# Performance work log

Measured on AMD Instinct MI355X. Metric: run time of the kernel, lower is better.

## Reference

```python
import jax, jax.numpy as jnp
import numpy as np

DROPOUT_P = 0.5
HALF_D_LOG_2PI = 8.0  # 0.5 * D * log(2*pi) constant from source, D=16


def _dropout(key, x, p):
    keep = 1.0 - p
    mask = jax.random.bernoulli(key, keep, x.shape).astype(x.dtype)
    return x * mask / keep


def _spmm(adj_vals, row, col, support, n):
    # out[i] = sum_{e: row[e]==i} adj_vals[e] * support[col[e]]
    return jax.ops.segment_sum(adj_vals[:, None] * support[col], row, num_segments=n)


def setup_inputs() -> dict:
    key = jax.random.key(0)
    ks = jax.random.split(key, 9)
    N, F_IN, D, C, E, K = 100000, 512, 16, 16, 3200000, 16
    return {
        "x": jax.random.normal(ks[0], (N, F_IN), dtype=jnp.float32),
        "W1": jax.random.normal(ks[1], (F_IN, D), dtype=jnp.float32) * 0.05,
        "W2": jax.random.normal(ks[2], (D, C), dtype=jnp.float32) * 0.2,
        "adj_vals": jax.random.uniform(ks[3], (E,), dtype=jnp.float32),
        "PI": jax.random.uniform(ks[4], (K,), dtype=jnp.float32, minval=0.01, maxval=1.0),
        "MUs": jax.random.normal(ks[5], (K, D), dtype=jnp.float32),
        "PREs": jax.random.uniform(ks[6], (K, D), dtype=jnp.float32, minval=0.1, maxval=1.0),
        "row": jnp.sort(jax.random.randint(ks[7], (E,), 0, N, dtype=jnp.int32)),
        "col": jax.random.randint(ks[8], (E,), 0, N, dtype=jnp.int32),
    }


def reference(x, W1, W2, adj_vals, PI, MUs, PREs, row, col):
    n = x.shape[0]
    dk1, dk2 = jax.random.split(jax.random.key(42))
    # layer 1: dropout -> linear (P1) -> spmm (P2)
    h = _spmm(adj_vals, row, col, _dropout(dk1, x, DROPOUT_P) @ W1, n)  # [N, D]
    # GMM log-likelihood: log N(h | MU_k, diag(1/PRE_k)) + log PI_k
    diff = h[:, None, :] - MUs[None, :, :]                      # [N, K, D]
    logcomp = (-0.5 * jnp.sum(diff * diff * PREs[None], axis=2)
               + jnp.log(PI)[None, :]
               + 0.5 * jnp.sum(jnp.log(PREs), axis=1)[None, :]
               - HALF_D_LOG_2PI * jnp.log(2.0 * jnp.pi))        # [N, K]
    probs = -jnp.mean(jnp.max(logcomp, axis=1))
    # layer 2: relu -> dropout -> linear -> spmm -> log_softmax
    x1 = jax.nn.relu(h)
    h2 = _spmm(adj_vals, row, col, _dropout(dk2, x1, DROPOUT_P) @ W2, n)  # [N, C]
    return jax.nn.log_softmax(h2, axis=1), probs
```

## Files before the change

### kernel.cpp

```cpp
#include <hip/hip_runtime.h>
#include <stdint.h>

typedef __attribute__((ext_vector_type(8))) short bf16x8;
typedef __attribute__((ext_vector_type(4))) float f32x4;
typedef __attribute__((ext_vector_type(4))) int i32x4;

__host__ __device__ __forceinline__ uint32_t rotl32(uint32_t x, int d){
  return (x << d) | (x >> (32 - d));
}

__host__ __device__ __forceinline__ void threefry2x32(uint32_t k0, uint32_t k1,
                                                      uint32_t x0, uint32_t x1,
                                                      uint32_t* o0, uint32_t* o1){
  uint32_t ks2 = k0 ^ k1 ^ 0x1BD11BDAu;
  x0 += k0; x1 += k1;
  x0 += x1; x1 = rotl32(x1,13); x1 ^= x0;
  x0 += x1; x1 = rotl32(x1,15); x1 ^= x0;
  x0 += x1; x1 = rotl32(x1,26); x1 ^= x0;
  x0 += x1; x1 = rotl32(x1, 6); x1 ^= x0;
  x0 += k1; x1 += ks2 + 1u;
  x0 += x1; x1 = rotl32(x1,17); x1 ^= x0;
  x0 += x1; x1 = rotl32(x1,29); x1 ^= x0;
  x0 += x1; x1 = rotl32(x1,16); x1 ^= x0;
  x0 += x1; x1 = rotl32(x1,24); x1 ^= x0;
  x0 += ks2; x1 += k0 + 2u;
  x0 += x1; x1 = rotl32(x1,13); x1 ^= x0;
  x0 += x1; x1 = rotl32(x1,15); x1 ^= x0;
  x0 += x1; x1 = rotl32(x1,26); x1 ^= x0;
  x0 += x1; x1 = rotl32(x1, 6); x1 ^= x0;
  x0 += k0; x1 += k1 + 3u;
  x0 += x1; x1 = rotl32(x1,17); x1 ^= x0;
  x0 += x1; x1 = rotl32(x1,29); x1 ^= x0;
  x0 += x1; x1 = rotl32(x1,16); x1 ^= x0;
  x0 += x1; x1 = rotl32(x1,24); x1 ^= x0;
  x0 += k1; x1 += ks2 + 4u;
  x0 += x1; x1 = rotl32(x1,13); x1 ^= x0;
  x0 += x1; x1 = rotl32(x1,15); x1 ^= x0;
  x0 += x1; x1 = rotl32(x1,26); x1 ^= x0;
  x0 += x1; x1 = rotl32(x1, 6); x1 ^= x0;
  x0 += ks2; x1 += k0 + 5u;
  *o0 = x0; *o1 = x1;
}

__device__ __forceinline__ uint32_t tf_dropbit(uint32_t k0, uint32_t k1, uint32_t j){
  uint32_t o0, o1;
  threefry2x32(k0, k1, 0u, j, &o0, &o1);
  return (o0 ^ o1) >> 31;
}

__device__ __forceinline__ uint32_t rotl1(uint32_t x, int d){
  return __builtin_amdgcn_alignbit(x, x, (uint32_t)(32 - d));
}

__device__ __forceinline__ ushort f2bf(float f){
  uint32_t u = __float_as_uint(f);
  u += 0x7FFFu + ((u >> 16) & 1u);
  return (ushort)(u >> 16);
}
__device__ __forceinline__ float bf2f(ushort b){
  return __uint_as_float(((uint32_t)b) << 16);
}
__device__ __forceinline__ uint32_t cvt_pk_bf16(float lo, float hi){
  uint32_t r;
  asm("v_cvt_pk_bf16_f32 %0, %1, %2" : "=v"(r) : "v"(lo), "v"(hi));
  return r;
}

__device__ __forceinline__ uint2 drop4(uint32_t k0, uint32_t k1, uint32_t j,
                                       float f0, float f1, float f2, float f3){
  uint32_t ks2 = k0 ^ k1 ^ 0x1BD11BDAu;
  uint32_t xa0 = k0, xa1 = (j + 0u) + k1;
  uint32_t xb0 = k0, xb1 = (j + 1u) + k1;
  uint32_t xc0 = k0, xc1 = (j + 2u) + k1;
  uint32_t xd0 = k0, xd1 = (j + 3u) + k1;
#define RR(d)                                              \
  xa0 += xa1; xa1 = rotl1(xa1, d); xa1 ^= xa0;             \
  xb0 += xb1; xb1 = rotl1(xb1, d); xb1 ^= xb0;             \
  xc0 += xc1; xc1 = rotl1(xc1, d); xc1 ^= xc0;             \
  xd0 += xd1; xd1 = rotl1(xd1, d); xd1 ^= xd0;
#define INJ(ka, kb)                                        \
  { uint32_t A = (ka), B = (kb);                           \
    xa0 += A; xa1 += B; xb0 += A; xb1 += B;                \
    xc0 += A; xc1 += B; xd0 += A; xd1 += B; }
  RR(13) RR(15) RR(26) RR(6)  INJ(k1, ks2 + 1u)
  RR(17) RR(29) RR(16) RR(24) INJ(ks2, k0 + 2u)
  RR(13) RR(15) RR(26) RR(6)  INJ(k0, k1 + 3u)
  RR(17) RR(29) RR(16) RR(24) INJ(k1, ks2 + 4u)
  RR(13) RR(15) RR(26) RR(6)  INJ(ks2, k0 + 5u)
#undef RR
#undef INJ
  uint32_t ba = xa0 ^ xa1, bb = xb0 ^ xb1, bc = xc0 ^ xc1, bd = xd0 ^ xd1;
  uint32_t sa = (uint32_t)((int32_t)ba >> 31);
  uint32_t sb = (uint32_t)((int32_t)bb >> 31);
  uint32_t sc = (uint32_t)((int32_t)bc >> 31);
  uint32_t sd = (uint32_t)((int32_t)bd >> 31);
  uint32_t v01 = cvt_pk_bf16(f0, f1);
  uint32_t v23 = cvt_pk_bf16(f2, f3);
  uint32_t m01 = __builtin_amdgcn_perm(sb, sa, 0x07060302u);
  uint32_t m23 = __builtin_amdgcn_perm(sd, sc, 0x07060302u);
  return make_uint2(v01 & ~m01, v23 & ~m23);
}

__global__ void k_prep(const float* __restrict__ W1, ushort* __restrict__ w1p,
                       const float* __restrict__ PI, const float* __restrict__ PREs,
                       float* __restrict__ ckg){
  int t = threadIdx.x;
  for (int u = 0; u < 32; ++u){
    int idx = u * 256 + t;
    int k = idx >> 4, c = idx & 15;
    w1p[((k >> 3) * 16 + c) * 8 + (k & 7)] = f2bf(2.0f * W1[idx]);
  }
  if (t < 16){
    float s = logf(PI[t]);
    #pragma unroll
    for (int j = 0; j < 16; ++j) s += 0.5f * logf(PREs[t * 16 + j]);
    ckg[t] = s - 8.0f * logf(6.28318530717958647692f);
  }
}

__global__ __launch_bounds__(256, 8) void k_main(
    const float* __restrict__ x, const ushort* __restrict__ w1p,
    ushort* __restrict__ s1, const int* __restrict__ rowv, int* __restrict__ rp,
    uint32_t dk0, uint32_t dk1, int N, int E, int nbG, int nbR){
  __shared__ float part[4][16][17];
  int bid = blockIdx.x;
  int m3 = bid % 3;
  if (m3 != 2){
    int rb = 2 * (bid / 3) + m3;
    if (rb < nbR){
      int e = rb * 256 + threadIdx.x;
      if (e <= E){
        int r0 = (e > 0) ? rowv[e - 1] : -1;
        int r1 = (e < E) ? rowv[e] : N;
        for (int r = r0 + 1; r <= r1; ++r) rp[r] = e;
      }
    }
    return;
  }
  int gb = bid / 3;
  if (gb >= nbG) return;

  int t = threadIdx.x;
  int l = t & 63, p = t >> 6;
  int rA = l & 15, kg = l >> 4;
  int r0 = gb * 16;
  int rr = r0 + rA; if (rr > N - 1) rr = N - 1;
  const float4* xv = reinterpret_cast<const float4*>(
      x + (size_t)rr * 512 + (p * 128 + kg * 8));
  uint32_t jb = (uint32_t)rr * 512u + (uint32_t)(p * 128 + kg * 8);

  const bf16x8* bp = reinterpret_cast<const bf16x8*>(w1p);
  bf16x8 Bf[4];
  #pragma unroll
  for (int q = 0; q < 4; ++q) Bf[q] = bp[((p * 4 + q) * 4 + kg) * 16 + rA];

  float4 xa = xv[0], xb = xv[1];
  __builtin_amdgcn_sched_barrier(0);

  f32x4 acc = {0.f, 0.f, 0.f, 0.f};
  #pragma unroll
  for (int ks = 0; ks < 4; ++ks){
    float4 na, nb;
    if (ks < 3){ na = xv[(ks + 1) * 8]; nb = xv[(ks + 1) * 8 + 1]; }
    __builtin_amdgcn_sched_barrier(0);
    uint32_t j0 = jb + (uint32_t)(ks * 32);
    uint2 lo = drop4(dk0, dk1, j0,      xa.x, xa.y, xa.z, xa.w);
    uint2 hi = drop4(dk0, dk1, j0 + 4u, xb.x, xb.y, xb.z, xb.w);
    i32x4 ai = {(int)lo.x, (int)lo.y, (int)hi.x, (int)hi.y};
    bf16x8 a = __builtin_bit_cast(bf16x8, ai);
    acc = __builtin_amdgcn_mfma_f32_16x16x32_bf16(a, Bf[ks], acc, 0, 0, 0);
    if (ks < 3){ xa = na; xb = nb; }
  }

  #pragma unroll
  for (int i2 = 0; i2 < 4; ++i2) part[p][kg * 4 + i2][rA] = acc[i2];
  __syncthreads();
  {
    int row = t >> 4, col = t & 15;
    int n = r0 + row;
    float sum = (part[0][row][col] + part[1][row][col])
              + (part[2][row][col] + part[3][row][col]);
    if (n < N) s1[(size_t)n * 16 + col] = f2bf(sum);
  }
}

__device__ __forceinline__ float edge_sum(const float* __restrict__ adj,
                                          const int* __restrict__ colv,
                                          const ushort* __restrict__ tbl_d,
                                          int e0, int e1){
  float hs = 0.f;
  int e = e0;
  int ea = (e0 + 3) & ~3; if (ea > e1) ea = e1;
  for (; e < ea; ++e) hs += adj[e] * bf2f(tbl_d[(size_t)colv[e] * 16]);
  float a0 = 0.f, a1 = 0.f, a2 = 0.f, a3 = 0.f;
  float b0 = 0.f, b1 = 0.f, b2 = 0.f, b3 = 0.f;
  for (; e + 8 <= e1; e += 8){
    float4 av = *reinterpret_cast<const float4*>(adj + e);
    int4   cv = *reinterpret_cast<const int4*>(colv + e);
    float4 aw = *reinterpret_cast<const float4*>(adj + e + 4);
    int4   cw = *reinterpret_cast<const int4*>(colv + e + 4);
    a0 += av.x * bf2f(tbl_d[(size_t)cv.x * 16]);
    a1 += av.y * bf2f(tbl_d[(size_t)cv.y * 16]);
    a2 += av.z * bf2f(tbl_d[(size_t)cv.z * 16]);
    a3 += av.w * bf2f(tbl_d[(size_t)cv.w * 16]);
    b0 += aw.x * bf2f(tbl_d[(size_t)cw.x * 16]);
    b1 += aw.y * bf2f(tbl_d[(size_t)cw.y * 16]);
    b2 += aw.z * bf2f(tbl_d[(size_t)cw.z * 16]);
    b3 += aw.w * bf2f(tbl_d[(size_t)cw.w * 16]);
  }
  if (e + 4 <= e1){
    float4 av = *reinterpret_cast<const float4*>(adj + e);
    int4   cv = *reinterpret_cast<const int4*>(colv + e);
    a0 += av.x * bf2f(tbl_d[(size_t)cv.x * 16]);
    a1 += av.y * bf2f(tbl_d[(size_t)cv.y * 16]);
    a2 += av.z * bf2f(tbl_d[(size_t)cv.z * 16]);
    a3 += av.w * bf2f(tbl_d[(size_t)cv.w * 16]);
    e += 4;
  }
  for (; e < e1; ++e) hs += adj[e] * bf2f(tbl_d[(size_t)colv[e] * 16]);
  return hs + ((a0 + b0) + (a1 + b1)) + ((a2 + b2) + (a3 + b3));
}

__global__ __launch_bounds__(256) void k_spmm1(
    const float* __restrict__ adj, const int* __restrict__ colv,
    const int* __restrict__ rp, const ushort* __restrict__ s1,
    const float* __restrict__ MUs, const float* __restrict__ PREs,
    const float* __restrict__ W2, const float* __restrict__ ckg,
    ushort* __restrict__ s2, float* __restrict__ partials,
    uint32_t dk0, uint32_t dk1, int N){
  __shared__ float muT[256], preT[256], w2s[256], ck[16];
  __shared__ float bsum;
  int t = threadIdx.x;
  {
    int j = t >> 4, k = t & 15;
    muT[t]  = MUs[k * 16 + j];
    preT[t] = PREs[k * 16 + j];
  }
  w2s[t] = W2[t];
  if (t < 16) ck[t] = ckg[t];
  if (t == 0) bsum = 0.f;
  __syncthreads();

  int i = blockIdx.x * 16 + (t >> 4);
  int d = t & 15;
  int base = t & 48;
  float h = 0.f;
  if (i < N) h = edge_sum(adj, colv, s1 + d, rp[i], rp[i + 1]);

  float lc = ck[d];
  #pragma unroll
  for (int j = 0; j < 16; ++j){
    float hj = __shfl(h, base + j, 64);
    float df = hj - muT[j * 16 + d];
    lc -= 0.5f * df * df * preT[j * 16 + d];
  }
  float m = lc;
  #pragma unroll
  for (int s = 1; s < 16; s <<= 1) m = fmaxf(m, __shfl_xor(m, s, 64));
  float mrow = (d == 0 && i < N) ? m : 0.f;
  mrow += __shfl_xor(mrow, 16, 64);
  mrow += __shfl_xor(mrow, 32, 64);
  if ((t & 63) == 0) atomicAdd(&bsum, mrow);

  float v = fmaxf(h, 0.f);
  float xd2 = (i < N && !tf_dropbit(dk0, dk1, (uint32_t)i * 16u + (uint32_t)d))
              ? 2.0f * v : 0.f;
  float s2v = 0.f;
  #pragma unroll
  for (int j = 0; j < 16; ++j)
    s2v += __shfl(xd2, base + j, 64) * w2s[j * 16 + d];
  if (i < N) s2[(size_t)i * 16 + d] = f2bf(s2v);
  __syncthreads();
  if (t == 0) partials[blockIdx.x] = bsum;
}

__global__ __launch_bounds__(256) void k_spmm2(
    const float* __restrict__ adj, const int* __restrict__ colv,
    const int* __restrict__ rp, const ushort* __restrict__ s2,
    const float* __restrict__ partials, int nparts,
    float* __restrict__ out, int N){
  int t = threadIdx.x;
  int i = blockIdx.x * 16 + (t >> 4);
  int d = t & 15;
  float h = 0.f;
  if (i < N) h = edge_sum(adj, colv, s2 + d, rp[i], rp[i + 1]);
  float m = h;
  #pragma unroll
  for (int s = 1; s < 16; s <<= 1) m = fmaxf(m, __shfl_xor(m, s, 64));
  float ex = expf(h - m);
  float ssum = ex;
  #pragma unroll
  for (int s = 1; s < 16; s <<= 1) ssum += __shfl_xor(ssum, s, 64);
  if (i < N) out[(size_t)i * 16 + d] = (h - m) - logf(ssum);

  if (blockIdx.x == 0){
    __shared__ float wsum[4];
    float s = 0.f;
    for (int q = t; q < nparts; q += 256) s += partials[q];
    #pragma unroll
    for (int sh = 1; sh < 64; sh <<= 1) s += __shfl_xor(s, sh, 64);
    if ((t & 63) == 0) wsum[t >> 6] = s;
    __syncthreads();
    if (t == 0)
      out[(size_t)N * 16] = -(wsum[0] + wsum[1] + wsum[2] + wsum[3]) / (float)N;
  }
}

extern "C" void kernel_launch(void* const* d_in, const int* in_sizes, int n_in,
                              void* d_out, int out_size, void* d_ws, size_t ws_size,
                              hipStream_t stream){
  const float* x    = (const float*)d_in[0];
  const float* W1   = (const float*)d_in[1];
  const float* W2   = (const float*)d_in[2];
  const float* adj  = (const float*)d_in[3];
  const float* PI   = (const float*)d_in[4];
  const float* MUs  = (const float*)d_in[5];
  const float* PREs = (const float*)d_in[6];
  const int*   rowv = (const int*)d_in[7];
  const int*   colv = (const int*)d_in[8];
  const int N = in_sizes[0] / 512;
  const int E = in_sizes[3];
  float* out = (float*)d_out;

  char* ws = (char*)d_ws;
  float* ckg = (float*)ws;
  int*   rp  = (int*)(ws + 256);
  size_t rpBytes = (((size_t)(N + 1) * 4) + 255) & ~(size_t)255;
  ushort* s1 = (ushort*)(ws + 256 + rpBytes);
  size_t s1Bytes = (((size_t)N * 16 * 2) + 255) & ~(size_t)255;
  ushort* s2 = (ushort*)(ws + 256 + rpBytes + s1Bytes);
  size_t s2Bytes = s1Bytes;
  float* partials = (float*)(ws + 256 + rpBytes + s1Bytes + s2Bytes);
  size_t pBytes = ((((size_t)N / 16 + 1) * 4) + 255) & ~(size_t)255;
  ushort* w1p = (ushort*)(ws + 256 + rpBytes + s1Bytes + s2Bytes + pBytes);

  uint32_t d10, d11, d20, d21;
  threefry2x32(0u, 42u, 0u, 0u, &d10, &d11);
  threefry2x32(0u, 42u, 0u, 1u, &d20, &d21);

  k_prep<<<1, 256, 0, stream>>>(W1, w1p, PI, PREs, ckg);

  int nbG = N / 16;
  int nbR = (E + 1 + 255) / 256;
  int grid = 3 * nbG;
  while (2 * ((grid - 1) / 3) + ((grid - 1) % 3 == 2 ? 0 : (grid - 1) % 3) < nbR - 1)
    ++grid;
  k_main<<<grid, 256, 0, stream>>>(x, w1p, s1, rowv, rp, d10, d11, N, E, nbG, nbR);

  int nb2 = (N + 15) / 16;
  k_spmm1<<<nb2, 256, 0, stream>>>(adj, colv, rp, s1, MUs, PREs, W2, ckg,
                                   s2, partials, d20, d21, N);
  k_spmm2<<<nb2, 256, 0, stream>>>(adj, colv, rp, s2, partials, nb2, out, N);
}
```

Baseline: 196.1 us.

## Use 512-thread GEMM blocks and split each row's edges across four lane groups in SpMM

k_main now runs 512-thread blocks. Each of 8 waves covers 64 of the K columns with two MFMAs, and the interleaved row-pointer blocks each handle 512 edges. The SpMM kernels switch from one row per 16 lanes to one row per wave: four 16-lane groups take strided edges and are combined with cross-lane shuffles. The aim is more memory-level parallelism per row on the ~32-edge rows, at the cost of more blocks, redundant GMM/W2 work in the upper lanes, and a larger partials array.

```diff
diff --git a/kernel.cpp b/kernel.cpp
--- a/kernel.cpp
+++ b/kernel.cpp
@@ -118,17 +118,16 @@
   }
 }
 
-__global__ __launch_bounds__(256, 8) void k_main(
+__global__ __launch_bounds__(512, 8) void k_main(
     const float* __restrict__ x, const ushort* __restrict__ w1p,
     ushort* __restrict__ s1, const int* __restrict__ rowv, int* __restrict__ rp,
     uint32_t dk0, uint32_t dk1, int N, int E, int nbG, int nbR){
-  __shared__ float part[4][16][17];
+  __shared__ float part[8][16][17];
   int bid = blockIdx.x;
-  int m3 = bid % 3;
-  if (m3 != 2){
-    int rb = 2 * (bid / 3) + m3;
+  if (!(bid & 1)){
+    int rb = bid >> 1;
     if (rb < nbR){
-      int e = rb * 256 + threadIdx.x;
+      int e = rb * 512 + threadIdx.x;
       if (e <= E){
         int r0 = (e > 0) ? rowv[e - 1] : -1;
         int r1 = (e < E) ? rowv[e] : N;
@@ -137,7 +136,7 @@
     }
     return;
   }
-  int gb = bid / 3;
+  int gb = bid >> 1;
   if (gb >= nbG) return;
 
   int t = threadIdx.x;
@@ -146,79 +145,44 @@
   int r0 = gb * 16;
   int rr = r0 + rA; if (rr > N - 1) rr = N - 1;
   const float4* xv = reinterpret_cast<const float4*>(
-      x + (size_t)rr * 512 + (p * 128 + kg * 8));
-  uint32_t jb = (uint32_t)rr * 512u + (uint32_t)(p * 128 + kg * 8);
+      x + (size_t)rr * 512 + (p * 64 + kg * 8));
+  uint32_t jb = (uint32_t)rr * 512u + (uint32_t)(p * 64 + kg * 8);
 
   const bf16x8* bp = reinterpret_cast<const bf16x8*>(w1p);
-  bf16x8 Bf[4];
-  #pragma unroll
-  for (int q = 0; q < 4; ++q) Bf[q] = bp[((p * 4 + q) * 4 + kg) * 16 + rA];
-
+  bf16x8 B0 = bp[((p * 2 + 0) * 4 + kg) * 16 + rA];
+  bf16x8 B1 = bp[((p * 2 + 1) * 4 + kg) * 16 + rA];
   float4 xa = xv[0], xb = xv[1];
+  float4 xc = xv[8], xd = xv[9];
   __builtin_amdgcn_sched_barrier(0);
 
   f32x4 acc = {0.f, 0.f, 0.f, 0.f};
-  #pragma unroll
-  for (int ks = 0; ks < 4; ++ks){
-    float4 na, nb;
-    if (ks < 3){ na = xv[(ks + 1) * 8]; nb = xv[(ks + 1) * 8 + 1]; }
-    __builtin_amdgcn_sched_barrier(0);
-    uint32_t j0 = jb + (uint32_t)(ks * 32);
-    uint2 lo = drop4(dk0, dk1, j0,      xa.x, xa.y, xa.z, xa.w);
-    uint2 hi = drop4(dk0, dk1, j0 + 4u, xb.x, xb.y, xb.z, xb.w);
+  {
+    uint2 lo = drop4(dk0, dk1, jb,      xa.x, xa.y, xa.z, xa.w);
+    uint2 hi = drop4(dk0, dk1, jb + 4u, xb.x, xb.y, xb.z, xb.w);
     i32x4 ai = {(int)lo.x, (int)lo.y, (int)hi.x, (int)hi.y};
-    bf16x8 a = __builtin_bit_cast(bf16x8, ai);
-    acc = __builtin_amdgcn_mfma_f32_16x16x32_bf16(a, Bf[ks], acc, 0, 0, 0);
-    if (ks < 3){ xa = na; xb = nb; }
+    acc = __builtin_amdgcn_mfma_f32_16x16x32_bf16(
+        __builtin_bit_cast(bf16x8, ai), B0, acc, 0, 0, 0);
+  }
+  {
+    uint2 lo = drop4(dk0, dk1, jb + 32u, xc.x, xc.y, xc.z, xc.w);
+    uint2 hi = drop4(dk0, dk1, jb + 36u, xd.x, xd.y, xd.z, xd.w);
+    i32x4 ai = {(int)lo.x, (int)lo.y, (int)hi.x, (int)hi.y};
+    acc = __builtin_amdgcn_mfma_f32_16x16x32_bf16(
+        __builtin_bit_cast(bf16x8, ai), B1, acc, 0, 0, 0);
   }
 
   #pragma unroll
   for (int i2 = 0; i2 < 4; ++i2) part[p][kg * 4 + i2][rA] = acc[i2];
   __syncthreads();
-  {
+  if (t < 256){
     int row = t >> 4, col = t & 15;
     int n = r0 + row;
-    float sum = (part[0][row][col] + part[1][row][col])
-              + (part[2][row][col] + part[3][row][col]);
+    float sum = ((part[0][row][col] + part[1][row][col])
+               + (part[2][row][col] + part[3][row][col]))
+              + ((part[4][row][col] + part[5][row][col])
+               + (part[6][row][col] + part[7][row][col]));
     if (n < N) s1[(size_t)n * 16 + col] = f2bf(sum);
   }
-}
-
-__device__ __forceinline__ float edge_sum(const float* __restrict__ adj,
-                                          const int* __restrict__ colv,
-                                          const ushort* __restrict__ tbl_d,
-                                          int e0, int e1){
-  float hs = 0.f;
-  int e = e0;
-  int ea = (e0 + 3) & ~3; if (ea > e1) ea = e1;
-  for (; e < ea; ++e) hs += adj[e] * bf2f(tbl_d[(size_t)colv[e] * 16]);
-  float a0 = 0.f, a1 = 0.f, a2 = 0.f, a3 = 0.f;
-  float b0 = 0.f, b1 = 0.f, b2 = 0.f, b3 = 0.f;
-  for (; e + 8 <= e1; e += 8){
-    float4 av = *reinterpret_cast<const float4*>(adj + e);
-    int4   cv = *reinterpret_cast<const int4*>(colv + e);
-    float4 aw = *reinterpret_cast<const float4*>(adj + e + 4);
-    int4   cw = *reinterpret_cast<const int4*>(colv + e + 4);
-    a0 += av.x * bf2f(tbl_d[(size_t)cv.x * 16]);
-    a1 += av.y * bf2f(tbl_d[(size_t)cv.y * 16]);
-    a2 += av.z * bf2f(tbl_d[(size_t)cv.z * 16]);
-    a3 += av.w * bf2f(tbl_d[(size_t)cv.w * 16]);
-    b0 += aw.x * bf2f(tbl_d[(size_t)cw.x * 16]);
-    b1 += aw.y * bf2f(tbl_d[(size_t)cw.y * 16]);
-    b2 += aw.z * bf2f(tbl_d[(size_t)cw.z * 16]);
-    b3 += aw.w * bf2f(tbl_d[(size_t)cw.w * 16]);
-  }
-  if (e + 4 <= e1){
-    float4 av = *reinterpret_cast<const float4*>(adj + e);
-    int4   cv = *reinterpret_cast<const int4*>(colv + e);
-    a0 += av.x * bf2f(tbl_d[(size_t)cv.x * 16]);
-    a1 += av.y * bf2f(tbl_d[(size_t)cv.y * 16]);
-    a2 += av.z * bf2f(tbl_d[(size_t)cv.z * 16]);
-    a3 += av.w * bf2f(tbl_d[(size_t)cv.w * 16]);
-    e += 4;
-  }
-  for (; e < e1; ++e) hs += adj[e] * bf2f(tbl_d[(size_t)colv[e] * 16]);
-  return hs + ((a0 + b0) + (a1 + b1)) + ((a2 + b2) + (a3 + b3));
 }
 
 __global__ __launch_bounds__(256) void k_spmm1(
@@ -241,26 +205,36 @@
   if (t == 0) bsum = 0.f;
   __syncthreads();
 
-  int i = blockIdx.x * 16 + (t >> 4);
-  int d = t & 15;
-  int base = t & 48;
+  int l = t & 63, w = t >> 6;
+  int d = l & 15, esub = l >> 4;
+  int i = blockIdx.x * 4 + w;
   float h = 0.f;
-  if (i < N) h = edge_sum(adj, colv, s1 + d, rp[i], rp[i + 1]);
+  if (i < N){
+    int e0 = rp[i], e1 = rp[i + 1];
+    const ushort* s1d = s1 + d;
+    float ha = 0.f, hb = 0.f;
+    int e = e0 + esub;
+    for (; e + 4 < e1; e += 8){
+      ha += adj[e]     * bf2f(s1d[(size_t)colv[e]     * 16]);
+      hb += adj[e + 4] * bf2f(s1d[(size_t)colv[e + 4] * 16]);
+    }
+    if (e < e1) ha += adj[e] * bf2f(s1d[(size_t)colv[e] * 16]);
+    h = ha + hb;
+  }
+  h += __shfl_xor(h, 16, 64);
+  h += __shfl_xor(h, 32, 64);
 
   float lc = ck[d];
   #pragma unroll
   for (int j = 0; j < 16; ++j){
-    float hj = __shfl(h, base + j, 64);
+    float hj = __shfl(h, j, 16);
     float df = hj - muT[j * 16 + d];
     lc -= 0.5f * df * df * preT[j * 16 + d];
   }
   float m = lc;
   #pragma unroll
-  for (int s = 1; s < 16; s <<= 1) m = fmaxf(m, __shfl_xor(m, s, 64));
-  float mrow = (d == 0 && i < N) ? m : 0.f;
-  mrow += __shfl_xor(mrow, 16, 64);
-  mrow += __shfl_xor(mrow, 32, 64);
-  if ((t & 63) == 0) atomicAdd(&bsum, mrow);
+  for (int s = 1; s < 16; s <<= 1) m = fmaxf(m, __shfl_xor(m, s, 16));
+  if (l == 0 && i < N) atomicAdd(&bsum, m);
 
   float v = fmaxf(h, 0.f);
   float xd2 = (i < N && !tf_dropbit(dk0, dk1, (uint32_t)i * 16u + (uint32_t)d))
@@ -268,8 +242,8 @@
   float s2v = 0.f;
   #pragma unroll
   for (int j = 0; j < 16; ++j)
-    s2v += __shfl(xd2, base + j, 64) * w2s[j * 16 + d];
-  if (i < N) s2[(size_t)i * 16 + d] = f2bf(s2v);
+    s2v += __shfl(xd2, j, 16) * w2s[j * 16 + d];
+  if (i < N && l < 16) s2[(size_t)i * 16 + d] = f2bf(s2v);
   __syncthreads();
   if (t == 0) partials[blockIdx.x] = bsum;
 }
@@ -280,18 +254,32 @@
     const float* __restrict__ partials, int nparts,
     float* __restrict__ out, int N){
   int t = threadIdx.x;
-  int i = blockIdx.x * 16 + (t >> 4);
-  int d = t & 15;
+  int l = t & 63, w = t >> 6;
+  int d = l & 15, esub = l >> 4;
+  int i = blockIdx.x * 4 + w;
   float h = 0.f;
-  if (i < N) h = edge_sum(adj, colv, s2 + d, rp[i], rp[i + 1]);
+  if (i < N){
+    int e0 = rp[i], e1 = rp[i + 1];
+    const ushort* s2d = s2 + d;
+    float ha = 0.f, hb = 0.f;
+    int e = e0 + esub;
+    for (; e + 4 < e1; e += 8){
+      ha += adj[e]     * bf2f(s2d[(size_t)colv[e]     * 16]);
+      hb += adj[e + 4] * bf2f(s2d[(size_t)colv[e + 4] * 16]);
+    }
+    if (e < e1) ha += adj[e] * bf2f(s2d[(size_t)colv[e] * 16]);
+    h = ha + hb;
+  }
+  h += __shfl_xor(h, 16, 64);
+  h += __shfl_xor(h, 32, 64);
   float m = h;
   #pragma unroll
-  for (int s = 1; s < 16; s <<= 1) m = fmaxf(m, __shfl_xor(m, s, 64));
+  for (int s = 1; s < 16; s <<= 1) m = fmaxf(m, __shfl_xor(m, s, 16));
   float ex = expf(h - m);
   float ssum = ex;
   #pragma unroll
-  for (int s = 1; s < 16; s <<= 1) ssum += __shfl_xor(ssum, s, 64);
-  if (i < N) out[(size_t)i * 16 + d] = (h - m) - logf(ssum);
+  for (int s = 1; s < 16; s <<= 1) ssum += __shfl_xor(ssum, s, 16);
+  if (i < N && l < 16) out[(size_t)i * 16 + d] = (h - m) - logf(ssum);
 
   if (blockIdx.x == 0){
     __shared__ float wsum[4];
@@ -331,7 +319,7 @@
   ushort* s2 = (ushort*)(ws + 256 + rpBytes + s1Bytes);
   size_t s2Bytes = s1Bytes;
   float* partials = (float*)(ws + 256 + rpBytes + s1Bytes + s2Bytes);
-  size_t pBytes = ((((size_t)N / 16 + 1) * 4) + 255) & ~(size_t)255;
+  size_t pBytes = ((((size_t)N / 4 + 1) * 4) + 255) & ~(size_t)255;
   ushort* w1p = (ushort*)(ws + 256 + rpBytes + s1Bytes + s2Bytes + pBytes);
 
   uint32_t d10, d11, d20, d21;
@@ -341,13 +329,11 @@
   k_prep<<<1, 256, 0, stream>>>(W1, w1p, PI, PREs, ckg);
 
   int nbG = N / 16;
-  int nbR = (E + 1 + 255) / 256;
-  int grid = 3 * nbG;
-  while (2 * ((grid - 1) / 3) + ((grid - 1) % 3 == 2 ? 0 : (grid - 1) % 3) < nbR - 1)
-    ++grid;
-  k_main<<<grid, 256, 0, stream>>>(x, w1p, s1, rowv, rp, d10, d11, N, E, nbG, nbR);
-
-  int nb2 = (N + 15) / 16;
+  int nbR = (E + 1 + 511) / 512;
+  int grid = 2 * ((nbG > nbR ? nbG : nbR)) + 2;
+  k_main<<<grid, 512, 0, stream>>>(x, w1p, s1, rowv, rp, d10, d11, N, E, nbG, nbR);
+
+  int nb2 = (N + 3) / 4;
   k_spmm1<<<nb2, 256, 0, stream>>>(adj, colv, rp, s1, MUs, PREs, W2, ckg,
                                    s2, partials, d20, d21, N);
   k_spmm2<<<nb2, 256, 0, stream>>>(adj, colv, rp, s2, partials, nb2, out, N);
```

Measured after the change: 336.0 us. 1.71x slower.
